# Kernel optimization log

Measured on AMD Instinct MI355X. Metric: run time of the kernel, lower is better.

Reference implementation:

```python
import jax, jax.numpy as jnp
import numpy as np

N_NODES = 100000

def _gcn_layer(x, W, b, src, dst, n):
    # x: [N, Fin], W: [Fin, Fout], b: [Fout]; edges src->dst, [E]
    h = x @ W  # [N, Fout]
    # add self loops
    loops = jnp.arange(n, dtype=src.dtype)
    s = jnp.concatenate([src, loops])
    d = jnp.concatenate([dst, loops])
    # symmetric GCN normalization: deg^{-1/2}[s] * deg^{-1/2}[d]
    deg = jax.ops.segment_sum(jnp.ones_like(d, dtype=h.dtype), d, num_segments=n)
    dis = jnp.where(deg > 0, jax.lax.rsqrt(jnp.maximum(deg, 1.0)), 0.0)
    norm = dis[s] * dis[d]  # [E+N]
    msg = h[s] * norm[:, None]  # [E+N, Fout]
    out = jax.ops.segment_sum(msg, d, num_segments=n)  # [N, Fout]
    return out + b


def setup_inputs() -> dict:
    key = jax.random.key(0)
    k1, k2, k3, k4, k5 = jax.random.split(key, 5)
    in_feat, hidden, out_feat = 64, 128, 64
    n_edges = 1600000
    node_features = jax.random.normal(k1, (N_NODES, in_feat), dtype=jnp.float32)
    edge_index = jax.random.randint(k2, (2, n_edges), 0, N_NODES, dtype=jnp.int32)
    # glorot-ish params
    W1 = jax.random.normal(k3, (in_feat, hidden), dtype=jnp.float32) * (1.0 / np.sqrt(in_feat))
    b1 = jnp.zeros((hidden,), dtype=jnp.float32)
    W2 = jax.random.normal(k4, (hidden, out_feat), dtype=jnp.float32) * (1.0 / np.sqrt(hidden))
    b2 = jnp.zeros((out_feat,), dtype=jnp.float32)
    return {"node_features": node_features, "edge_index": edge_index,
            "W1": W1, "b1": b1, "W2": W2, "b2": b2}


def reference(node_features, edge_index, W1, b1, W2, b2):
    src, dst = edge_index[0], edge_index[1]
    n = node_features.shape[0]
    h = _gcn_layer(node_features, W1, b1, src, dst, n)
    h = jax.nn.relu(h)
    h = _gcn_layer(h, W2, b2, src, dst, n)
    return h
```

## Files before the change

kernel.cpp:

```cpp
#include <hip/hip_runtime.h>
#include <hip/hip_fp16.h>

#define NN 100000
#define NB 391
#define NG 512
#define REGION 6144

using f16x8 = __attribute__((ext_vector_type(8))) _Float16;
using f32x4 = __attribute__((ext_vector_type(4))) float;

__global__ __launch_bounds__(256) void bhist_kernel(const int* __restrict__ dst,
                                                    int* __restrict__ counts, int E) {
    __shared__ int h[NB];
    for (int i = threadIdx.x; i < NB; i += 256) h[i] = 0;
    __syncthreads();
    const int g = blockIdx.x;
    const int chunk = (E + NG - 1) / NG;
    const int lo = g * chunk, hi = min(E, lo + chunk);
    for (int e = lo + threadIdx.x; e < hi; e += 256) atomicAdd(&h[dst[e] >> 8], 1);
    __syncthreads();
    for (int i = threadIdx.x; i < NB; i += 256) counts[g * NB + i] = h[i];
}

__global__ __launch_bounds__(256) void bprefix_kernel(int* __restrict__ counts,
                                                      int* __restrict__ btot,
                                                      const float* __restrict__ W1,
                                                      const float* __restrict__ W2,
                                                      __half* __restrict__ W1t,
                                                      __half* __restrict__ W2t) {
    const int b = blockIdx.x, t = threadIdx.x;
    if (b == NB) {
        for (int i = t; i < 64 * 128; i += 256) {
            int k = i / 128, c = i % 128;
            W1t[c * 64 + k] = __float2half(W1[i]);
            int k2 = i / 64, c2 = i % 64;
            W2t[c2 * 128 + k2] = __float2half(W2[i]);
        }
        return;
    }
    __shared__ int sm[256];
    int loc[NG / 256];
    int s = 0;
    #pragma unroll
    for (int p = 0; p < NG / 256; ++p) {
        loc[p] = counts[((NG / 256) * t + p) * NB + b];
        s += loc[p];
    }
    sm[t] = s; __syncthreads();
    for (int off = 1; off < 256; off <<= 1) {
        int x = (t >= off) ? sm[t - off] : 0; __syncthreads();
        sm[t] += x; __syncthreads();
    }
    int run = b * REGION + sm[t] - s;
    #pragma unroll
    for (int p = 0; p < NG / 256; ++p) {
        int c = loc[p];
        counts[((NG / 256) * t + p) * NB + b] = run;
        run += c;
    }
    if (t == 255) btot[b] = sm[255];
}

__global__ __launch_bounds__(256) void bscatter_kernel(const int* __restrict__ src,
                                                       const int* __restrict__ dst,
                                                       const int* __restrict__ cstart,
                                                       int* __restrict__ staging, int E) {
    __shared__ int cur[NB];
    const int g = blockIdx.x;
    for (int i = threadIdx.x; i < NB; i += 256) cur[i] = cstart[g * NB + i];
    __syncthreads();
    const int chunk = (E + NG - 1) / NG;
    const int lo = g * chunk, hi = min(E, lo + chunk);
    for (int e = lo + threadIdx.x; e < hi; e += 256) {
        int d = dst[e];
        int pos = atomicAdd(&cur[d >> 8], 1);
        staging[pos] = src[e] | ((d & 255) << 17);
    }
}

__global__ __launch_bounds__(256) void bfinal_kernel(const int* __restrict__ btot,
                                                     const int* __restrict__ staging,
                                                     int* __restrict__ csr,
                                                     int* __restrict__ row_beg,
                                                     int* __restrict__ row_end,
                                                     float* __restrict__ dis,
                                                     const float* __restrict__ x,
                                                     __half* __restrict__ xh,
                                                     int N) {
    __shared__ int h[256];
    __shared__ int sc[256];
    __shared__ int cur[256];
    __shared__ float sdis[256];
    const int b = blockIdx.x, t = threadIdx.x;
    const int base = b * REGION;
    const int endb = base + btot[b];
    h[t] = 0; __syncthreads();
    for (int i = base + t; i < endb; i += 256) atomicAdd(&h[staging[i] >> 17], 1);
    __syncthreads();
    int v = h[t];
    sc[t] = v; __syncthreads();
    for (int off = 1; off < 256; off <<= 1) {
        int xv = (t >= off) ? sc[t - off] : 0; __syncthreads();
        sc[t] += xv; __syncthreads();
    }
    int excl = sc[t] - v;
    cur[t] = base + excl;
    float dv = rsqrtf((float)v + 1.0f);
    sdis[t] = dv;
    int node = b * 256 + t;
    if (node < N) {
        row_beg[node] = base + excl;
        row_end[node] = base + excl + v;
        dis[node] = dv;
    }
    __syncthreads();
    for (int i = base + t; i < endb; i += 256) {
        int p = staging[i];
        int pos = atomicAdd(&cur[p >> 17], 1);
        csr[pos] = p & 0x1FFFF;
    }
    const int node0 = b * 256;
    const int nmax = min(256, N - node0);
    for (int i = t; i < nmax * 16; i += 256) {
        int nl = i >> 4, c4 = i & 15;
        float4 vx = ((const float4*)x)[(size_t)(node0 + nl) * 16 + c4];
        float wq = sdis[nl];
        __half2* o = (__half2*)&xh[(size_t)(node0 + nl) * 64 + c4 * 4];
        o[0] = __floats2half2_rn(vx.x * wq, vx.y * wq);
        o[1] = __floats2half2_rn(vx.z * wq, vx.w * wq);
    }
}

__global__ __launch_bounds__(512) void gfuse_kernel(const __half* __restrict__ tab,
                                                    const float* __restrict__ dis,
                                                    const __half* __restrict__ W1t,
                                                    const float* __restrict__ b1,
                                                    const __half* __restrict__ W2t,
                                                    const int* __restrict__ row_beg,
                                                    const int* __restrict__ row_end,
                                                    const int* __restrict__ csr,
                                                    __half* __restrict__ zh, int N,
                                                    float one) {
    __shared__ _Float16 sA[16][72];
    __shared__ _Float16 sH[16][136];
    __shared__ float sP[4][16][16];
    const int tid = threadIdx.x;
    const int nodeL = tid >> 5;
    const int l32 = tid & 31;
    const int e = l32 >> 3;
    const int sub = l32 & 7;
    const int node0 = blockIdx.x * 16;
    const int node = node0 + nodeL;
    const int beg = row_beg[node], end = row_end[node];

    float acc[8];
    {
        f16x8 sv = *reinterpret_cast<const f16x8*>(&tab[(size_t)node * 64 + sub * 8]);
        #pragma unroll
        for (int q = 0; q < 8; ++q) acc[q] = (e == 0) ? (float)sv[q] : 0.0f;
    }
    for (int j = beg + e; j < end; j += 4) {
        int s = csr[j];
        f16x8 v = *reinterpret_cast<const f16x8*>(&tab[(size_t)s * 64 + sub * 8]);
        #pragma unroll
        for (int q = 0; q < 8; ++q) acc[q] = fmaf((float)v[q], one, acc[q]);
    }
    #pragma unroll
    for (int q = 0; q < 8; ++q) {
        acc[q] += __shfl_xor(acc[q], 8);
        acc[q] += __shfl_xor(acc[q], 16);
    }
    if (e == 0) {
        const float dd = dis[node];
        f16x8 o;
        #pragma unroll
        for (int q = 0; q < 8; ++q) o[q] = (_Float16)(acc[q] * dd);
        *reinterpret_cast<f16x8*>(&sA[nodeL][sub * 8]) = o;
    }
    __syncthreads();

    const int w = tid >> 6, lane = tid & 63;
    const int lrow = lane & 15, kgrp = lane >> 4;
    {
        const int col = w * 16 + lrow;
        f32x4 a1 = (f32x4){0.f, 0.f, 0.f, 0.f};
        #pragma unroll
        for (int ks = 0; ks < 2; ++ks) {
            const int kbase = ks * 32 + kgrp * 8;
            f16x8 a  = *reinterpret_cast<const f16x8*>(&sA[lrow][kbase]);
            f16x8 bf = *reinterpret_cast<const f16x8*>(&W1t[(size_t)col * 64 + kbase]);
            a1 = __builtin_amdgcn_mfma_f32_16x16x32_f16(a, bf, a1, 0, 0, 0);
        }
        const float bb = b1[col];
        #pragma unroll
        for (int r = 0; r < 4; ++r) {
            const int row = kgrp * 4 + r;
            sH[row][col] = (_Float16)fmaxf(a1[r] + bb, 0.0f);
        }
    }
    __syncthreads();
    {
        const int t2 = w & 3, kh = w >> 2;
        const int col = t2 * 16 + lrow;
        f32x4 a2 = (f32x4){0.f, 0.f, 0.f, 0.f};
        #pragma unroll
        for (int ks = 0; ks < 2; ++ks) {
            const int kbase = kh * 64 + ks * 32 + kgrp * 8;
            f16x8 a  = *reinterpret_cast<const f16x8*>(&sH[lrow][kbase]);
            f16x8 bf = *reinterpret_cast<const f16x8*>(&W2t[(size_t)col * 128 + kbase]);
            a2 = __builtin_amdgcn_mfma_f32_16x16x32_f16(a, bf, a2, 0, 0, 0);
        }
        if (kh == 1) {
            #pragma unroll
            for (int r = 0; r < 4; ++r) sP[t2][kgrp * 4 + r][lrow] = a2[r];
        }
        __syncthreads();
        if (kh == 0) {
            #pragma unroll
            for (int r = 0; r < 4; ++r) {
                const int row = kgrp * 4 + r;
                float v = (a2[r] + sP[t2][row][lrow]) * dis[node0 + row];
                zh[(size_t)(node0 + row) * 64 + col] = __float2half(v);
            }
        }
    }
}

__global__ __launch_bounds__(256) void gather2_kernel(const __half* __restrict__ tab,
                                                      const float* __restrict__ dis,
                                                      const float* __restrict__ b,
                                                      const int* __restrict__ row_beg,
                                                      const int* __restrict__ row_end,
                                                      const int* __restrict__ csr,
                                                      float* __restrict__ out, int N,
                                                      float one) {
    const int node = blockIdx.x * 4 + (threadIdx.x >> 6);
    const int lane = threadIdx.x & 63;
    const int g   = lane >> 3;
    const int sub = lane & 7;
    if (node >= N) return;
    const int beg = row_beg[node], end = row_end[node];

    float acc[8];
    {
        f16x8 sv = *reinterpret_cast<const f16x8*>(&tab[(size_t)node * 64 + sub * 8]);
        #pragma unroll
        for (int q = 0; q < 8; ++q) acc[q] = (g == 0) ? (float)sv[q] : 0.0f;
    }
    int j = beg;
    for (; j + 16 <= end; j += 16) {
        int sA = csr[j + g];
        int sB = csr[j + 8 + g];
        f16x8 vA = *reinterpret_cast<const f16x8*>(&tab[(size_t)sA * 64 + sub * 8]);
        f16x8 vB = *reinterpret_cast<const f16x8*>(&tab[(size_t)sB * 64 + sub * 8]);
        #pragma unroll
        for (int q = 0; q < 8; ++q) acc[q] = fmaf((float)vA[q], one, acc[q]);
        #pragma unroll
        for (int q = 0; q < 8; ++q) acc[q] = fmaf((float)vB[q], one, acc[q]);
    }
    if (j + 8 <= end) {
        int s = csr[j + g];
        f16x8 v = *reinterpret_cast<const f16x8*>(&tab[(size_t)s * 64 + sub * 8]);
        #pragma unroll
        for (int q = 0; q < 8; ++q) acc[q] = fmaf((float)v[q], one, acc[q]);
        j += 8;
    }
    if (j + g < end) {
        int s = csr[j + g];
        f16x8 v = *reinterpret_cast<const f16x8*>(&tab[(size_t)s * 64 + sub * 8]);
        #pragma unroll
        for (int q = 0; q < 8; ++q) acc[q] = fmaf((float)v[q], one, acc[q]);
    }
    #pragma unroll
    for (int q = 0; q < 8; ++q) {
        acc[q] += __shfl_xor(acc[q], 8);
        acc[q] += __shfl_xor(acc[q], 16);
        acc[q] += __shfl_xor(acc[q], 32);
    }
    if (g == 0) {
        const float dd = dis[node];
        float vv[8];
        #pragma unroll
        for (int q = 0; q < 8; ++q) vv[q] = acc[q] * dd + b[sub * 8 + q];
        float* op = &out[(size_t)node * 64 + sub * 8];
        *reinterpret_cast<float4*>(op)     = make_float4(vv[0], vv[1], vv[2], vv[3]);
        *reinterpret_cast<float4*>(op + 4) = make_float4(vv[4], vv[5], vv[6], vv[7]);
    }
}

extern "C" void kernel_launch(void* const* d_in, const int* in_sizes, int n_in,
                              void* d_out, int out_size, void* d_ws, size_t ws_size,
                              hipStream_t stream) {
    const float* x  = (const float*)d_in[0];
    const int*   ei = (const int*)d_in[1];
    const float* W1 = (const float*)d_in[2];
    const float* b1 = (const float*)d_in[3];
    const float* W2 = (const float*)d_in[4];
    const float* b2 = (const float*)d_in[5];
    float* out = (float*)d_out;

    const int N = NN;
    const int E = in_sizes[1] / 2;
    const int* src = ei;
    const int* dst = ei + E;

    int* counts   = (int*)d_ws;
    int* btot     = counts + NG * NB;
    int* row_beg  = btot + 512;
    int* row_end  = row_beg + N;
    float* dis    = (float*)(row_end + N);
    int* staging  = (int*)(dis + N);
    int* csr      = staging + (size_t)NB * REGION;
    float* base   = (float*)(csr + (size_t)NB * REGION);
    __half* xh    = (__half*)base;
    __half* zh    = (__half*)(base + (size_t)N * 32);
    __half* W1t   = (__half*)(base + (size_t)N * 64);
    __half* W2t   = W1t + 128 * 64;

    bhist_kernel<<<NG, 256, 0, stream>>>(dst, counts, E);
    bprefix_kernel<<<NB + 1, 256, 0, stream>>>(counts, btot, W1, W2, W1t, W2t);
    bscatter_kernel<<<NG, 256, 0, stream>>>(src, dst, counts, staging, E);
    bfinal_kernel<<<NB, 256, 0, stream>>>(btot, staging, csr, row_beg, row_end, dis, x, xh, N);

    gfuse_kernel<<<N / 16, 512, 0, stream>>>(xh, dis, W1t, b1, W2t, row_beg, row_end, csr, zh, N, 1.0f);

    gather2_kernel<<<N / 4, 256, 0, stream>>>(zh, dis, b2, row_beg, row_end, csr, out, N, 1.0f);
}
```

Baseline: 166.3 us.

## Fuse bucket histogram, prefix and scatter into one kernel with global atomic cursors

Replaces the three-kernel bucket sort (per-block histogram, cross-block prefix scan, scatter) with one kernel. Each block stages its dst chunk in shared memory, builds a local histogram, reserves space per bucket with a global atomicAdd on a zeroed cursor array, then scatters. This cuts two launches and the counts-matrix round trip, and reads dst once instead of twice. The cost is a memset and nondeterministic edge order within each bucket. The shared-memory padding of sH in gfuse also changes from 136 to 132.

```diff
diff --git a/kernel.cpp b/kernel.cpp
--- a/kernel.cpp
+++ b/kernel.cpp
@@ -3,33 +3,23 @@
 
 #define NN 100000
 #define NB 391
-#define NG 512
+#define NG2 512
+#define CH 3136
 #define REGION 6144
 
 using f16x8 = __attribute__((ext_vector_type(8))) _Float16;
 using f32x4 = __attribute__((ext_vector_type(4))) float;
 
-__global__ __launch_bounds__(256) void bhist_kernel(const int* __restrict__ dst,
-                                                    int* __restrict__ counts, int E) {
-    __shared__ int h[NB];
-    for (int i = threadIdx.x; i < NB; i += 256) h[i] = 0;
-    __syncthreads();
-    const int g = blockIdx.x;
-    const int chunk = (E + NG - 1) / NG;
-    const int lo = g * chunk, hi = min(E, lo + chunk);
-    for (int e = lo + threadIdx.x; e < hi; e += 256) atomicAdd(&h[dst[e] >> 8], 1);
-    __syncthreads();
-    for (int i = threadIdx.x; i < NB; i += 256) counts[g * NB + i] = h[i];
-}
-
-__global__ __launch_bounds__(256) void bprefix_kernel(int* __restrict__ counts,
-                                                      int* __restrict__ btot,
-                                                      const float* __restrict__ W1,
-                                                      const float* __restrict__ W2,
-                                                      __half* __restrict__ W1t,
-                                                      __half* __restrict__ W2t) {
-    const int b = blockIdx.x, t = threadIdx.x;
-    if (b == NB) {
+__global__ __launch_bounds__(256) void bsort2_kernel(const int* __restrict__ src,
+                                                     const int* __restrict__ dst,
+                                                     int* __restrict__ cursor,
+                                                     int* __restrict__ staging, int E,
+                                                     const float* __restrict__ W1,
+                                                     const float* __restrict__ W2,
+                                                     __half* __restrict__ W1t,
+                                                     __half* __restrict__ W2t) {
+    const int g = blockIdx.x, t = threadIdx.x;
+    if (g == NG2) {
         for (int i = t; i < 64 * 128; i += 256) {
             int k = i / 128, c = i % 128;
             W1t[c * 64 + k] = __float2half(W1[i]);
@@ -38,43 +28,27 @@
         }
         return;
     }
-    __shared__ int sm[256];
-    int loc[NG / 256];
-    int s = 0;
-    #pragma unroll
-    for (int p = 0; p < NG / 256; ++p) {
-        loc[p] = counts[((NG / 256) * t + p) * NB + b];
-        s += loc[p];
-    }
-    sm[t] = s; __syncthreads();
-    for (int off = 1; off < 256; off <<= 1) {
-        int x = (t >= off) ? sm[t - off] : 0; __syncthreads();
-        sm[t] += x; __syncthreads();
-    }
-    int run = b * REGION + sm[t] - s;
-    #pragma unroll
-    for (int p = 0; p < NG / 256; ++p) {
-        int c = loc[p];
-        counts[((NG / 256) * t + p) * NB + b] = run;
-        run += c;
-    }
-    if (t == 255) btot[b] = sm[255];
-}
-
-__global__ __launch_bounds__(256) void bscatter_kernel(const int* __restrict__ src,
-                                                       const int* __restrict__ dst,
-                                                       const int* __restrict__ cstart,
-                                                       int* __restrict__ staging, int E) {
+    __shared__ int sdst[CH];
+    __shared__ int h[NB];
     __shared__ int cur[NB];
-    const int g = blockIdx.x;
-    for (int i = threadIdx.x; i < NB; i += 256) cur[i] = cstart[g * NB + i];
-    __syncthreads();
-    const int chunk = (E + NG - 1) / NG;
-    const int lo = g * chunk, hi = min(E, lo + chunk);
-    for (int e = lo + threadIdx.x; e < hi; e += 256) {
-        int d = dst[e];
+    const int chunk = (E + NG2 - 1) / NG2;
+    const int lo = g * chunk;
+    const int n = min(E - lo, chunk);
+    for (int i = t; i < n; i += 256) sdst[i] = dst[lo + i];
+    for (int i = t; i < NB; i += 256) h[i] = 0;
+    __syncthreads();
+    for (int i = t; i < n; i += 256) atomicAdd(&h[sdst[i] >> 8], 1);
+    __syncthreads();
+    for (int i = t; i < NB; i += 256) {
+        int c = h[i];
+        int base = (c > 0) ? atomicAdd(&cursor[i], c) : 0;
+        cur[i] = i * REGION + base;
+    }
+    __syncthreads();
+    for (int i = t; i < n; i += 256) {
+        int d = sdst[i];
         int pos = atomicAdd(&cur[d >> 8], 1);
-        staging[pos] = src[e] | ((d & 255) << 17);
+        staging[pos] = src[lo + i] | ((d & 255) << 17);
     }
 }
 
@@ -142,7 +116,7 @@
                                                     __half* __restrict__ zh, int N,
                                                     float one) {
     __shared__ _Float16 sA[16][72];
-    __shared__ _Float16 sH[16][136];
+    __shared__ _Float16 sH[16][132];
     __shared__ float sP[4][16][16];
     const int tid = threadIdx.x;
     const int nodeL = tid >> 5;
@@ -304,9 +278,8 @@
     const int* src = ei;
     const int* dst = ei + E;
 
-    int* counts   = (int*)d_ws;
-    int* btot     = counts + NG * NB;
-    int* row_beg  = btot + 512;
+    int* cursor   = (int*)d_ws;
+    int* row_beg  = cursor + 512;
     int* row_end  = row_beg + N;
     float* dis    = (float*)(row_end + N);
     int* staging  = (int*)(dis + N);
@@ -317,10 +290,9 @@
     __half* W1t   = (__half*)(base + (size_t)N * 64);
     __half* W2t   = W1t + 128 * 64;
 
-    bhist_kernel<<<NG, 256, 0, stream>>>(dst, counts, E);
-    bprefix_kernel<<<NB + 1, 256, 0, stream>>>(counts, btot, W1, W2, W1t, W2t);
-    bscatter_kernel<<<NG, 256, 0, stream>>>(src, dst, counts, staging, E);
-    bfinal_kernel<<<NB, 256, 0, stream>>>(btot, staging, csr, row_beg, row_end, dis, x, xh, N);
+    hipMemsetAsync(cursor, 0, NB * sizeof(int), stream);
+    bsort2_kernel<<<NG2 + 1, 256, 0, stream>>>(src, dst, cursor, staging, E, W1, W2, W1t, W2t);
+    bfinal_kernel<<<NB, 256, 0, stream>>>(cursor, staging, csr, row_beg, row_end, dis, x, xh, N);
 
     gfuse_kernel<<<N / 16, 512, 0, stream>>>(xh, dis, W1t, b1, W2t, row_beg, row_end, csr, zh, N, 1.0f);
 
```

New measurement: 169.2 us. Within noise of the previous version (+1.7%).

## Bin nodes by degree so fused layer-1 blocks process similar-degree nodes

Applied to the files above, without the earlier changes.

Nodes are bucketed by in-degree (capped at 63) during CSR finalization. A new tiny kernel builds a tile map from bin counts, and the fused gather+MLP kernel takes its 16 nodes per block from one degree bin. This aims to cut load imbalance within a block, where the slowest node's gather sets the pace for the block-wide MFMA stage. The cost is an extra launch, scattered output writes, more global atomics, and padded tiles with idle rows at bin boundaries.

```diff
diff --git a/kernel.cpp b/kernel.cpp
--- a/kernel.cpp
+++ b/kernel.cpp
@@ -5,12 +5,16 @@
 #define NB 391
 #define NG 512
 #define REGION 6144
+#define BINCAP 16384
+#define GRID_T 6314
 
 using f16x8 = __attribute__((ext_vector_type(8))) _Float16;
 using f32x4 = __attribute__((ext_vector_type(4))) float;
 
 __global__ __launch_bounds__(256) void bhist_kernel(const int* __restrict__ dst,
-                                                    int* __restrict__ counts, int E) {
+                                                    int* __restrict__ counts,
+                                                    int* __restrict__ bincur, int E) {
+    if (blockIdx.x == 0 && threadIdx.x < 64) bincur[threadIdx.x] = threadIdx.x * BINCAP;
     __shared__ int h[NB];
     for (int i = threadIdx.x; i < NB; i += 256) h[i] = 0;
     __syncthreads();
@@ -86,15 +90,20 @@
                                                      float* __restrict__ dis,
                                                      const float* __restrict__ x,
                                                      __half* __restrict__ xh,
+                                                     int* __restrict__ bincur,
+                                                     int* __restrict__ order,
                                                      int N) {
     __shared__ int h[256];
     __shared__ int sc[256];
     __shared__ int cur[256];
     __shared__ float sdis[256];
+    __shared__ int bh[64], lbase[64], lcnt[64];
     const int b = blockIdx.x, t = threadIdx.x;
     const int base = b * REGION;
     const int endb = base + btot[b];
-    h[t] = 0; __syncthreads();
+    h[t] = 0;
+    if (t < 64) { bh[t] = 0; lcnt[t] = 0; }
+    __syncthreads();
     for (int i = base + t; i < endb; i += 256) atomicAdd(&h[staging[i] >> 17], 1);
     __syncthreads();
     int v = h[t];
@@ -108,10 +117,12 @@
     float dv = rsqrtf((float)v + 1.0f);
     sdis[t] = dv;
     int node = b * 256 + t;
+    int bin = -1;
     if (node < N) {
         row_beg[node] = base + excl;
         row_end[node] = base + excl + v;
         dis[node] = dv;
+        bin = min(v, 63);
     }
     __syncthreads();
     for (int i = base + t; i < endb; i += 256) {
@@ -129,6 +140,41 @@
         o[0] = __floats2half2_rn(vx.x * wq, vx.y * wq);
         o[1] = __floats2half2_rn(vx.z * wq, vx.w * wq);
     }
+    if (bin >= 0) atomicAdd(&bh[bin], 1);
+    __syncthreads();
+    if (t < 64) {
+        int c = bh[t];
+        lbase[t] = (c > 0) ? atomicAdd(&bincur[t], c) : 0;
+    }
+    __syncthreads();
+    if (bin >= 0) {
+        int p = lbase[bin] + atomicAdd(&lcnt[bin], 1);
+        order[p] = node;
+    }
+}
+
+__global__ __launch_bounds__(256) void tmap_kernel(const int* __restrict__ bincur,
+                                                   int* __restrict__ tmap, int grid) {
+    __shared__ int nt[64], ps[65];
+    const int t = threadIdx.x;
+    if (t < 64) nt[t] = (bincur[t] - t * BINCAP + 15) >> 4;
+    __syncthreads();
+    if (t == 0) {
+        int s = 0;
+        for (int b2 = 0; b2 < 64; ++b2) { ps[b2] = s; s += nt[b2]; }
+        ps[64] = s;
+    }
+    __syncthreads();
+    const int T = ps[64];
+    for (int i = t; i < grid; i += 256) {
+        int val = -1;
+        if (i < T) {
+            int bin = 0;
+            for (int b2 = 1; b2 < 64; ++b2) if (i >= ps[b2]) bin = b2;
+            val = (bin << 16) | (i - ps[bin]);
+        }
+        tmap[i] = val;
+    }
 }
 
 __global__ __launch_bounds__(512) void gfuse_kernel(const __half* __restrict__ tab,
@@ -139,18 +185,30 @@
                                                     const int* __restrict__ row_beg,
                                                     const int* __restrict__ row_end,
                                                     const int* __restrict__ csr,
+                                                    const int* __restrict__ bincur,
+                                                    const int* __restrict__ order,
+                                                    const int* __restrict__ tmap,
                                                     __half* __restrict__ zh, int N,
                                                     float one) {
+    const int tm = tmap[blockIdx.x];
+    if (tm < 0) return;
+    const int bin = tm >> 16, ti = tm & 0xFFFF;
+    const int fill = bincur[bin] - bin * BINCAP;
+    const int tbase = ti * 16;
+
     __shared__ _Float16 sA[16][72];
-    __shared__ _Float16 sH[16][136];
+    __shared__ _Float16 sH[16][132];
     __shared__ float sP[4][16][16];
+    __shared__ int snode[16];
+    __shared__ float sdis16[16];
     const int tid = threadIdx.x;
     const int nodeL = tid >> 5;
     const int l32 = tid & 31;
     const int e = l32 >> 3;
     const int sub = l32 & 7;
-    const int node0 = blockIdx.x * 16;
-    const int node = node0 + nodeL;
+    const int nl_ok = (tbase + nodeL) < fill;
+    const int node = order[bin * BINCAP + tbase + (nl_ok ? nodeL : 0)];
+    if (l32 == 0) { snode[nodeL] = node; sdis16[nodeL] = dis[node]; }
     const int beg = row_beg[node], end = row_end[node];
 
     float acc[8];
@@ -219,8 +277,11 @@
             #pragma unroll
             for (int r = 0; r < 4; ++r) {
                 const int row = kgrp * 4 + r;
-                float v = (a2[r] + sP[t2][row][lrow]) * dis[node0 + row];
-                zh[(size_t)(node0 + row) * 64 + col] = __float2half(v);
+                if (tbase + row < fill) {
+                    int nd = snode[row];
+                    float vv = (a2[r] + sP[t2][row][lrow]) * sdis16[row];
+                    zh[(size_t)nd * 64 + col] = __float2half(vv);
+                }
             }
         }
     }
@@ -306,10 +367,13 @@
 
     int* counts   = (int*)d_ws;
     int* btot     = counts + NG * NB;
-    int* row_beg  = btot + 512;
+    int* bincur   = btot + 512;
+    int* tmap     = bincur + 256;
+    int* row_beg  = tmap + 8192;
     int* row_end  = row_beg + N;
     float* dis    = (float*)(row_end + N);
-    int* staging  = (int*)(dis + N);
+    int* order    = (int*)(dis + N);
+    int* staging  = order + 64 * BINCAP;
     int* csr      = staging + (size_t)NB * REGION;
     float* base   = (float*)(csr + (size_t)NB * REGION);
     __half* xh    = (__half*)base;
@@ -317,12 +381,14 @@
     __half* W1t   = (__half*)(base + (size_t)N * 64);
     __half* W2t   = W1t + 128 * 64;
 
-    bhist_kernel<<<NG, 256, 0, stream>>>(dst, counts, E);
+    bhist_kernel<<<NG, 256, 0, stream>>>(dst, counts, bincur, E);
     bprefix_kernel<<<NB + 1, 256, 0, stream>>>(counts, btot, W1, W2, W1t, W2t);
     bscatter_kernel<<<NG, 256, 0, stream>>>(src, dst, counts, staging, E);
-    bfinal_kernel<<<NB, 256, 0, stream>>>(btot, staging, csr, row_beg, row_end, dis, x, xh, N);
-
-    gfuse_kernel<<<N / 16, 512, 0, stream>>>(xh, dis, W1t, b1, W2t, row_beg, row_end, csr, zh, N, 1.0f);
+    bfinal_kernel<<<NB, 256, 0, stream>>>(btot, staging, csr, row_beg, row_end, dis, x, xh, bincur, order, N);
+    tmap_kernel<<<1, 256, 0, stream>>>(bincur, tmap, GRID_T);
+
+    gfuse_kernel<<<GRID_T, 512, 0, stream>>>(xh, dis, W1t, b1, W2t, row_beg, row_end, csr,
+                                             bincur, order, tmap, zh, N, 1.0f);
 
     gather2_kernel<<<N / 4, 256, 0, stream>>>(zh, dis, b2, row_beg, row_end, csr, out, N, 1.0f);
 }
```

Result: slower. 184.7 us (+11.1%).

## Give each node a full wavefront in fused GCN layer kernel with split-K MFMA

Applied to the files above, without the earlier changes.

The fused aggregation+MLP kernel now launches 1024 threads per 16-node block, so each node gets a whole 64-lane wavefront. The 8 lane groups gather neighbours, unrolled two edges at a time, instead of 4 groups in a half-wave. Both small GEMMs are split along K across all 16 waves, with partial sums combined through shared memory, and dis is cached in LDS. The aim is more memory-level parallelism on the irregular gathers, at the cost of more barriers, more shared memory and lower block-level occupancy from the 1024-thread blocks.

```diff
diff --git a/kernel.cpp b/kernel.cpp
--- a/kernel.cpp
+++ b/kernel.cpp
@@ -131,36 +131,55 @@
     }
 }
 
-__global__ __launch_bounds__(512) void gfuse_kernel(const __half* __restrict__ tab,
-                                                    const float* __restrict__ dis,
-                                                    const __half* __restrict__ W1t,
-                                                    const float* __restrict__ b1,
-                                                    const __half* __restrict__ W2t,
-                                                    const int* __restrict__ row_beg,
-                                                    const int* __restrict__ row_end,
-                                                    const int* __restrict__ csr,
-                                                    __half* __restrict__ zh, int N,
-                                                    float one) {
+__global__ __launch_bounds__(1024) void gfuse_kernel(const __half* __restrict__ tab,
+                                                     const float* __restrict__ dis,
+                                                     const __half* __restrict__ W1t,
+                                                     const float* __restrict__ b1,
+                                                     const __half* __restrict__ W2t,
+                                                     const int* __restrict__ row_beg,
+                                                     const int* __restrict__ row_end,
+                                                     const int* __restrict__ csr,
+                                                     __half* __restrict__ zh, int N,
+                                                     float one) {
     __shared__ _Float16 sA[16][72];
-    __shared__ _Float16 sH[16][136];
-    __shared__ float sP[4][16][16];
+    __shared__ _Float16 sH[16][132];
+    __shared__ float sP[12][16][16];
+    __shared__ float sdis16[16];
     const int tid = threadIdx.x;
-    const int nodeL = tid >> 5;
-    const int l32 = tid & 31;
-    const int e = l32 >> 3;
-    const int sub = l32 & 7;
+    const int wv = tid >> 6;
+    const int lane = tid & 63;
+    const int g   = lane >> 3;
+    const int sub = lane & 7;
     const int node0 = blockIdx.x * 16;
-    const int node = node0 + nodeL;
+    const int node = node0 + wv;
     const int beg = row_beg[node], end = row_end[node];
 
     float acc[8];
     {
         f16x8 sv = *reinterpret_cast<const f16x8*>(&tab[(size_t)node * 64 + sub * 8]);
         #pragma unroll
-        for (int q = 0; q < 8; ++q) acc[q] = (e == 0) ? (float)sv[q] : 0.0f;
-    }
-    for (int j = beg + e; j < end; j += 4) {
-        int s = csr[j];
+        for (int q = 0; q < 8; ++q) acc[q] = (g == 0) ? (float)sv[q] : 0.0f;
+    }
+    int j = beg;
+    for (; j + 16 <= end; j += 16) {
+        int sA0 = csr[j + g];
+        int sB0 = csr[j + 8 + g];
+        f16x8 vA = *reinterpret_cast<const f16x8*>(&tab[(size_t)sA0 * 64 + sub * 8]);
+        f16x8 vB = *reinterpret_cast<const f16x8*>(&tab[(size_t)sB0 * 64 + sub * 8]);
+        #pragma unroll
+        for (int q = 0; q < 8; ++q) acc[q] = fmaf((float)vA[q], one, acc[q]);
+        #pragma unroll
+        for (int q = 0; q < 8; ++q) acc[q] = fmaf((float)vB[q], one, acc[q]);
+    }
+    if (j + 8 <= end) {
+        int s = csr[j + g];
+        f16x8 v = *reinterpret_cast<const f16x8*>(&tab[(size_t)s * 64 + sub * 8]);
+        #pragma unroll
+        for (int q = 0; q < 8; ++q) acc[q] = fmaf((float)v[q], one, acc[q]);
+        j += 8;
+    }
+    if (j + g < end) {
+        int s = csr[j + g];
         f16x8 v = *reinterpret_cast<const f16x8*>(&tab[(size_t)s * 64 + sub * 8]);
         #pragma unroll
         for (int q = 0; q < 8; ++q) acc[q] = fmaf((float)v[q], one, acc[q]);
@@ -169,59 +188,67 @@
     for (int q = 0; q < 8; ++q) {
         acc[q] += __shfl_xor(acc[q], 8);
         acc[q] += __shfl_xor(acc[q], 16);
-    }
-    if (e == 0) {
+        acc[q] += __shfl_xor(acc[q], 32);
+    }
+    if (g == 0) {
         const float dd = dis[node];
+        if (sub == 0) sdis16[wv] = dd;
         f16x8 o;
         #pragma unroll
         for (int q = 0; q < 8; ++q) o[q] = (_Float16)(acc[q] * dd);
-        *reinterpret_cast<f16x8*>(&sA[nodeL][sub * 8]) = o;
-    }
-    __syncthreads();
-
-    const int w = tid >> 6, lane = tid & 63;
+        *reinterpret_cast<f16x8*>(&sA[wv][sub * 8]) = o;
+    }
+    __syncthreads();
+
     const int lrow = lane & 15, kgrp = lane >> 4;
+    f32x4 a1;
+    const int ct1 = wv & 7, kh1 = wv >> 3;
     {
-        const int col = w * 16 + lrow;
-        f32x4 a1 = (f32x4){0.f, 0.f, 0.f, 0.f};
-        #pragma unroll
-        for (int ks = 0; ks < 2; ++ks) {
-            const int kbase = ks * 32 + kgrp * 8;
-            f16x8 a  = *reinterpret_cast<const f16x8*>(&sA[lrow][kbase]);
-            f16x8 bf = *reinterpret_cast<const f16x8*>(&W1t[(size_t)col * 64 + kbase]);
-            a1 = __builtin_amdgcn_mfma_f32_16x16x32_f16(a, bf, a1, 0, 0, 0);
-        }
+        const int col = ct1 * 16 + lrow;
+        const int kbase = kh1 * 32 + kgrp * 8;
+        f16x8 a  = *reinterpret_cast<const f16x8*>(&sA[lrow][kbase]);
+        f16x8 bf = *reinterpret_cast<const f16x8*>(&W1t[(size_t)col * 64 + kbase]);
+        a1 = (f32x4){0.f, 0.f, 0.f, 0.f};
+        a1 = __builtin_amdgcn_mfma_f32_16x16x32_f16(a, bf, a1, 0, 0, 0);
+        if (kh1 == 1) {
+            #pragma unroll
+            for (int r = 0; r < 4; ++r) sP[ct1][kgrp * 4 + r][lrow] = a1[r];
+        }
+    }
+    __syncthreads();
+    if (kh1 == 0) {
+        const int col = ct1 * 16 + lrow;
         const float bb = b1[col];
         #pragma unroll
         for (int r = 0; r < 4; ++r) {
             const int row = kgrp * 4 + r;
-            sH[row][col] = (_Float16)fmaxf(a1[r] + bb, 0.0f);
-        }
-    }
-    __syncthreads();
+            sH[row][col] = (_Float16)fmaxf(a1[r] + sP[ct1][row][lrow] + bb, 0.0f);
+        }
+    }
+    __syncthreads();
+
+    f32x4 a2;
+    const int ct2 = wv & 3, kq = wv >> 2;
     {
-        const int t2 = w & 3, kh = w >> 2;
-        const int col = t2 * 16 + lrow;
-        f32x4 a2 = (f32x4){0.f, 0.f, 0.f, 0.f};
-        #pragma unroll
-        for (int ks = 0; ks < 2; ++ks) {
-            const int kbase = kh * 64 + ks * 32 + kgrp * 8;
-            f16x8 a  = *reinterpret_cast<const f16x8*>(&sH[lrow][kbase]);
-            f16x8 bf = *reinterpret_cast<const f16x8*>(&W2t[(size_t)col * 128 + kbase]);
-            a2 = __builtin_amdgcn_mfma_f32_16x16x32_f16(a, bf, a2, 0, 0, 0);
-        }
-        if (kh == 1) {
+        const int col = ct2 * 16 + lrow;
+        const int kbase = kq * 32 + kgrp * 8;
+        f16x8 a  = *reinterpret_cast<const f16x8*>(&sH[lrow][kbase]);
+        f16x8 bf = *reinterpret_cast<const f16x8*>(&W2t[(size_t)col * 128 + kbase]);
+        a2 = (f32x4){0.f, 0.f, 0.f, 0.f};
+        a2 = __builtin_amdgcn_mfma_f32_16x16x32_f16(a, bf, a2, 0, 0, 0);
+        if (kq > 0) {
             #pragma unroll
-            for (int r = 0; r < 4; ++r) sP[t2][kgrp * 4 + r][lrow] = a2[r];
-        }
-        __syncthreads();
-        if (kh == 0) {
-            #pragma unroll
-            for (int r = 0; r < 4; ++r) {
-                const int row = kgrp * 4 + r;
-                float v = (a2[r] + sP[t2][row][lrow]) * dis[node0 + row];
-                zh[(size_t)(node0 + row) * 64 + col] = __float2half(v);
-            }
+            for (int r = 0; r < 4; ++r) sP[(kq - 1) * 4 + ct2][kgrp * 4 + r][lrow] = a2[r];
+        }
+    }
+    __syncthreads();
+    if (kq == 0) {
+        const int col = ct2 * 16 + lrow;
+        #pragma unroll
+        for (int r = 0; r < 4; ++r) {
+            const int row = kgrp * 4 + r;
+            float v = a2[r] + sP[ct2][row][lrow] + sP[4 + ct2][row][lrow] + sP[8 + ct2][row][lrow];
+            zh[(size_t)(node0 + row) * 64 + col] = __float2half(v * sdis16[row]);
         }
     }
 }
@@ -322,7 +349,7 @@
     bscatter_kernel<<<NG, 256, 0, stream>>>(src, dst, counts, staging, E);
     bfinal_kernel<<<NB, 256, 0, stream>>>(btot, staging, csr, row_beg, row_end, dis, x, xh, N);
 
-    gfuse_kernel<<<N / 16, 512, 0, stream>>>(xh, dis, W1t, b1, W2t, row_beg, row_end, csr, zh, N, 1.0f);
+    gfuse_kernel<<<N / 16, 1024, 0, stream>>>(xh, dis, W1t, b1, W2t, row_beg, row_end, csr, zh, N, 1.0f);
 
     gather2_kernel<<<N / 4, 256, 0, stream>>>(zh, dis, b2, row_beg, row_end, csr, out, N, 1.0f);
 }
```

After: 179.6 us. +8.0%, slower.
